# Kernel optimization log

Measured on AMD Instinct MI355X. Metric: run time of the kernel, lower is better.

## Reference

```python
import jax, jax.numpy as jnp
import numpy as np

N_SRC = 200000   # source (input) nodes
N_DST = 50000    # destination (output) nodes; dst node i == src node i (block convention)
E = 800000       # edges
IN = 256
OUT = 64
H = 3
SLOPE = 0.2      # leaky_relu negative_slope


def setup_inputs() -> dict:
    key = jax.random.key(0)
    k0, k1, k2, k3, k4, k5 = jax.random.split(key, 6)
    x = jax.random.normal(k0, (N_SRC, IN), dtype=jnp.float32)
    W = jax.random.normal(k1, (H * OUT, IN), dtype=jnp.float32) * (1.0 / np.sqrt(IN))
    attn_l = jax.random.normal(k2, (1, H, OUT), dtype=jnp.float32) * 0.1
    attn_r = jax.random.normal(k3, (1, H, OUT), dtype=jnp.float32) * 0.1
    src = jax.random.randint(k4, (E,), 0, N_SRC, dtype=jnp.int32)
    dst = jnp.sort(jax.random.randint(k5, (E,), 0, N_DST, dtype=jnp.int32))
    return {"x": x, "W": W, "attn_l": attn_l, "attn_r": attn_r, "src": src, "dst": dst}


def reference(x, W, attn_l, attn_r, src, dst):
    # fc + reshape to heads: [N_src, H, F]
    feat = (x @ W.T).reshape(N_SRC, H, OUT)
    # per-head attention logits
    el = jnp.sum(feat * attn_l, axis=-1)          # [N_src, H]
    er = jnp.sum(feat[:N_DST] * attn_r, axis=-1)  # [N_dst, H] (self_gather of out nodes)
    # edge scores: apply_edge + leaky_relu -> [E, H]
    e = jax.nn.leaky_relu(el[src] + er[dst], negative_slope=SLOPE)
    # segmented max over incoming edges of each dst node (gather_local_max)
    m = jax.ops.segment_max(e, dst, num_segments=N_DST)
    m = jnp.where(jnp.isfinite(m), m, jnp.float32(0))  # empty segments -> 0
    m = jax.lax.stop_gradient(m)
    ex = jnp.exp(e - m[dst])                       # [E, H]
    s = jax.ops.segment_sum(ex, dst, num_segments=N_DST)  # [N_dst, H]
    s = jnp.where(s == 0, jnp.float32(1), s)       # sum_exponent[sum==0] = 1
    att = ex / s[dst]                              # [E, H]
    # attention_gather: sum over edges of att * src feature -> [N_dst, H, F]
    out = jax.ops.segment_sum(att[:, :, None] * feat[src], dst, num_segments=N_DST)
    return out.reshape(N_DST, H * OUT)
```

## Files before the change

kernel.cpp:

```cpp
#include <hip/hip_runtime.h>
#include <hip/hip_bf16.h>

#define N_SRCN 200000
#define N_DSTN 50000
#define NEDGE 800000
#define KIN 256
#define NF 192
#define SLOPE 0.2f
#define TILES 6250
#define GBLK 512

typedef __attribute__((ext_vector_type(8))) short bf16x8;
typedef __attribute__((ext_vector_type(4))) float f32x4;

__device__ __forceinline__ unsigned short f2bf(float f) {
    union { float f; unsigned int u; } v; v.f = f;
    unsigned int u = v.u;
    return (unsigned short)((u + 0x7FFFu + ((u >> 16) & 1u)) >> 16);
}
__device__ __forceinline__ float bf2f(unsigned short h) {
    union { unsigned int u; float f; } v; v.u = ((unsigned int)h) << 16;
    return v.f;
}
__device__ __forceinline__ unsigned int cvt2(float lo, float hi) {
    __hip_bfloat162 h = __float22bfloat162_rn(float2{lo, hi});
    union { __hip_bfloat162 h; unsigned int u; } c; c.h = h;
    return c.u;
}
__device__ __forceinline__ void gl_lds16(const void* g, void* l) {
    __builtin_amdgcn_global_load_lds(
        (const __attribute__((address_space(1))) unsigned int*)g,
        (__attribute__((address_space(3))) unsigned int*)l, 16, 0, 0);
}

__global__ void prep_kernel(const float* __restrict__ W, unsigned short* __restrict__ Wp,
                            const int* __restrict__ dst, int* __restrict__ rp) {
    const int bid = blockIdx.x;
    if (bid < 24) {
        int tid = bid * 256 + threadIdx.x;
        if (tid >= 12 * 8 * 64) return;
        int lane = tid & 63;
        int g = tid >> 6;
        int nt = g % 12, ks = g / 12;
        int col = nt * 16 + (lane & 15);
        int k = ks * 32 + (lane >> 4) * 8;
        const float* wsrc = &W[col * KIN + k];
        unsigned short* o = &Wp[tid * 8];
        #pragma unroll
        for (int j = 0; j < 8; ++j) o[j] = f2bf(wsrc[j]);
    } else {
        int d = (bid - 24) * 256 + threadIdx.x;
        if (d > N_DSTN) return;
        int lo = 0, hi = NEDGE;
        while (lo < hi) {
            int mid = (lo + hi) >> 1;
            if (dst[mid] < d) lo = mid + 1; else hi = mid;
        }
        rp[d] = lo;
    }
}

__launch_bounds__(256, 2)
__global__ void gemm_feat(const float* __restrict__ x, const unsigned short* __restrict__ Wp,
                          const float* __restrict__ attn_l, const float* __restrict__ attn_r,
                          unsigned short* __restrict__ feat,
                          float* __restrict__ el4, float* __restrict__ er4) {
    __shared__ float Ab[2][32][256];
    __shared__ float parts[32][4][4][2];
    const int t = threadIdx.x;
    const int wid = t >> 6, lane = t & 63;
    const int al = lane & 15, ah = lane >> 4;

    bf16x8 bv[8][3];
    #pragma unroll
    for (int ks = 0; ks < 8; ++ks)
        #pragma unroll
        for (int j = 0; j < 3; ++j)
            bv[ks][j] = *(const bf16x8*)&Wp[(size_t)(ks * 12 + wid * 3 + j) * 512 + lane * 8];

    float Al[3], Ar[3];
    #pragma unroll
    for (int j = 0; j < 3; ++j) {
        Al[j] = attn_l[(wid * 3 + j) * 16 + al];
        Ar[j] = attn_r[(wid * 3 + j) * 16 + al];
    }

    #define STAGE(buf, tile)                                                     \
        {                                                                        \
            const int rbase = (tile) * 32;                                       \
            _Pragma("unroll")                                                    \
            for (int rr = 0; rr < 8; ++rr) {                                     \
                const int rl = wid * 8 + rr;                                     \
                const float* gp = &x[(size_t)(rbase + rl) * KIN +                \
                                     ((lane ^ (rl & 7)) << 2)];                  \
                gl_lds16(gp, &Ab[buf][rl][0]);                                   \
            }                                                                    \
        }

    STAGE(0, blockIdx.x)

    for (int tl = blockIdx.x, it = 0; tl < TILES; tl += GBLK, ++it) {
        const int cur = it & 1;
        if (tl + GBLK < TILES) {
            STAGE(cur ^ 1, tl + GBLK)
            asm volatile("s_waitcnt vmcnt(8)" ::: "memory");
        } else {
            asm volatile("s_waitcnt vmcnt(0)" ::: "memory");
        }
        __syncthreads();

        const int r0 = tl * 32;
        f32x4 acc[2][3] = {};
        #pragma unroll
        for (int ks = 0; ks < 8; ++ks) {
            #pragma unroll
            for (int rt = 0; rt < 2; ++rt) {
                const int row = rt * 16 + al;
                const int q0 = (ks * 8 + ah * 2);
                const int key = row & 7;
                const float4 v0 = *(const float4*)&Ab[cur][row][((q0 ^ key) << 2)];
                const float4 v1 = *(const float4*)&Ab[cur][row][(((q0 + 1) ^ key) << 2)];
                union { bf16x8 v; unsigned int u[4]; } av;
                av.u[0] = cvt2(v0.x, v0.y);
                av.u[1] = cvt2(v0.z, v0.w);
                av.u[2] = cvt2(v1.x, v1.y);
                av.u[3] = cvt2(v1.z, v1.w);
                #pragma unroll
                for (int j = 0; j < 3; ++j)
                    acc[rt][j] = __builtin_amdgcn_mfma_f32_16x16x32_bf16(av.v, bv[ks][j], acc[rt][j], 0, 0, 0);
            }
        }

        #pragma unroll
        for (int rt = 0; rt < 2; ++rt)
            #pragma unroll
            for (int j = 0; j < 3; ++j) {
                const int col = (wid * 3 + j) * 16 + al;
                #pragma unroll
                for (int e = 0; e < 4; ++e) {
                    const int row = r0 + rt * 16 + ah * 4 + e;
                    feat[(size_t)row * NF + col] = f2bf(acc[rt][j][e]);
                }
            }

        #pragma unroll
        for (int rt = 0; rt < 2; ++rt)
            #pragma unroll
            for (int e = 0; e < 4; ++e)
                #pragma unroll
                for (int j = 0; j < 3; ++j) {
                    float sl = acc[rt][j][e] * Al[j];
                    float sr = acc[rt][j][e] * Ar[j];
                    #pragma unroll
                    for (int m = 1; m <= 8; m <<= 1) {
                        sl += __shfl_xor(sl, m);
                        sr += __shfl_xor(sr, m);
                    }
                    if (al == 0) {
                        const int rloc = rt * 16 + ah * 4 + e;
                        const int nt = wid * 3 + j;
                        parts[rloc][nt >> 2][nt & 3][0] = sl;
                        parts[rloc][nt >> 2][nt & 3][1] = sr;
                    }
                }
        __syncthreads();

        if (t < 128) {
            const int rloc = t >> 2, h = t & 3;
            const int row = r0 + rloc;
            float sl = 0.f, sr = 0.f;
            if (h < 3) {
                sl = parts[rloc][h][0][0] + parts[rloc][h][1][0]
                   + parts[rloc][h][2][0] + parts[rloc][h][3][0];
                sr = parts[rloc][h][0][1] + parts[rloc][h][1][1]
                   + parts[rloc][h][2][1] + parts[rloc][h][3][1];
            }
            el4[(size_t)row * 4 + h] = sl;
            if (row < N_DSTN) er4[(size_t)row * 4 + h] = sr;
        }
    }
    #undef STAGE
}

__launch_bounds__(256)
__global__ void gather_kernel(const unsigned short* __restrict__ feat,
                              const float* __restrict__ el4, const float* __restrict__ er4,
                              const int* __restrict__ src, const int* __restrict__ rp,
                              float* __restrict__ out) {
    const int lane = threadIdx.x & 63;
    const int d = (blockIdx.x * blockDim.x + threadIdx.x) >> 6;
    if (d >= N_DSTN) return;
    const int lo = rp[d], hi = rp[d + 1];
    const float4 erv = *(const float4*)&er4[(size_t)d * 4];

    float a0 = 0.f, a1 = 0.f, a2 = 0.f, s0 = 0.f, s1 = 0.f, s2 = 0.f;
    for (int base = lo; base < hi; base += 64) {
        const int cnt = min(64, hi - base);
        int sv = 0; float w0 = 0.f, w1 = 0.f, w2 = 0.f;
        if (lane < cnt) {
            sv = src[base + lane];
            const float4 elv = *(const float4*)&el4[(size_t)sv * 4];
            float e0 = elv.x + erv.x; e0 = e0 >= 0.f ? e0 : SLOPE * e0; w0 = __expf(e0);
            float e1 = elv.y + erv.y; e1 = e1 >= 0.f ? e1 : SLOPE * e1; w1 = __expf(e1);
            float e2 = elv.z + erv.z; e2 = e2 >= 0.f ? e2 : SLOPE * e2; w2 = __expf(e2);
        }
        int j = 0;
        for (; j + 8 <= cnt; j += 8) {
            unsigned short f0[8], f1[8], f2[8];
            float u0[8], u1[8], u2[8];
            #pragma unroll
            for (int q = 0; q < 8; ++q) {
                const int sj = __shfl(sv, j + q);
                const unsigned short* fp = &feat[(size_t)sj * NF + lane];
                f0[q] = fp[0]; f1[q] = fp[64]; f2[q] = fp[128];
                u0[q] = __shfl(w0, j + q);
                u1[q] = __shfl(w1, j + q);
                u2[q] = __shfl(w2, j + q);
            }
            #pragma unroll
            for (int q = 0; q < 8; ++q) {
                s0 += u0[q]; a0 += u0[q] * bf2f(f0[q]);
                s1 += u1[q]; a1 += u1[q] * bf2f(f1[q]);
                s2 += u2[q]; a2 += u2[q] * bf2f(f2[q]);
            }
        }
        for (; j < cnt; ++j) {
            const int sj = __shfl(sv, j);
            const float u0 = __shfl(w0, j);
            const float u1 = __shfl(w1, j);
            const float u2 = __shfl(w2, j);
            const unsigned short* fp = &feat[(size_t)sj * NF + lane];
            s0 += u0; a0 += u0 * bf2f(fp[0]);
            s1 += u1; a1 += u1 * bf2f(fp[64]);
            s2 += u2; a2 += u2 * bf2f(fp[128]);
        }
    }
    if (hi == lo) { s0 = 1.f; s1 = 1.f; s2 = 1.f; }
    float* op = &out[(size_t)d * NF];
    op[lane]       = a0 / s0;
    op[64 + lane]  = a1 / s1;
    op[128 + lane] = a2 / s2;
}

extern "C" void kernel_launch(void* const* d_in, const int* in_sizes, int n_in,
                              void* d_out, int out_size, void* d_ws, size_t ws_size,
                              hipStream_t stream) {
    const float* x      = (const float*)d_in[0];
    const float* W      = (const float*)d_in[1];
    const float* attn_l = (const float*)d_in[2];
    const float* attn_r = (const float*)d_in[3];
    const int*   src    = (const int*)d_in[4];
    const int*   dst    = (const int*)d_in[5];
    float* out = (float*)d_out;

    char* ws = (char*)d_ws;
    unsigned short* feat = (unsigned short*)ws;
    float* el4 = (float*)(ws + 76800000);
    float* er4 = (float*)(ws + 80000000);
    unsigned short* Wp = (unsigned short*)(ws + 80800000);
    int*   rp = (int*)(ws + 80898304);

    prep_kernel<<<24 + 196, 256, 0, stream>>>(W, Wp, dst, rp);
    gemm_feat<<<GBLK, 256, 0, stream>>>(x, Wp, attn_l, attn_r, feat, el4, er4);
    gather_kernel<<<12500, 256, 0, stream>>>(feat, el4, er4, src, rp, out);
}
```

Measured before the change: 177.4 us.

## Move GEMM weights to LDS and load x directly with 512-thread blocks

The feature GEMM is restructured. W fragments are now staged once per block into LDS instead of being held in registers. x rows are read straight from global memory into registers, replacing the double-buffered async LDS staging of x. Blocks grow to 512 threads (8 waves split into two row halves times four column groups), grid shrinks to 256 blocks, and the el/er reductions run as two separate LDS passes. The aim is to cut register pressure and raise occupancy, at the cost of the explicit prefetch pipeline for x and extra barriers.

Measured after the change: 277.4 us. 1.56x slower.

```diff
diff --git a/kernel.cpp b/kernel.cpp
--- a/kernel.cpp
+++ b/kernel.cpp
@@ -7,8 +7,8 @@
 #define KIN 256
 #define NF 192
 #define SLOPE 0.2f
-#define TILES 6250
-#define GBLK 512
+#define TILES32 6250
+#define GEMM_BLOCKS 256
 
 typedef __attribute__((ext_vector_type(8))) short bf16x8;
 typedef __attribute__((ext_vector_type(4))) float f32x4;
@@ -60,126 +60,114 @@
     }
 }
 
-__launch_bounds__(256, 2)
+__launch_bounds__(512, 2)
 __global__ void gemm_feat(const float* __restrict__ x, const unsigned short* __restrict__ Wp,
                           const float* __restrict__ attn_l, const float* __restrict__ attn_r,
                           unsigned short* __restrict__ feat,
                           float* __restrict__ el4, float* __restrict__ er4) {
-    __shared__ float Ab[2][32][256];
-    __shared__ float parts[32][4][4][2];
+    __shared__ unsigned short Bl[12 * 8 * 512];
+    __shared__ float parts[2][32][4][4];
     const int t = threadIdx.x;
     const int wid = t >> 6, lane = t & 63;
     const int al = lane & 15, ah = lane >> 4;
-
-    bf16x8 bv[8][3];
+    const int rh = wid >> 2;
+    const int j3 = wid & 3;
+
     #pragma unroll
-    for (int ks = 0; ks < 8; ++ks)
-        #pragma unroll
-        for (int j = 0; j < 3; ++j)
-            bv[ks][j] = *(const bf16x8*)&Wp[(size_t)(ks * 12 + wid * 3 + j) * 512 + lane * 8];
+    for (int i = 0; i < 12; ++i) {
+        const int gbase = i * 512 + wid * 64;
+        gl_lds16(&Wp[(size_t)(gbase + lane) * 8], &Bl[(size_t)gbase * 8]);
+    }
+    asm volatile("s_waitcnt vmcnt(0)" ::: "memory");
+    __syncthreads();
 
     float Al[3], Ar[3];
     #pragma unroll
-    for (int j = 0; j < 3; ++j) {
-        Al[j] = attn_l[(wid * 3 + j) * 16 + al];
-        Ar[j] = attn_r[(wid * 3 + j) * 16 + al];
-    }
-
-    #define STAGE(buf, tile)                                                     \
-        {                                                                        \
-            const int rbase = (tile) * 32;                                       \
-            _Pragma("unroll")                                                    \
-            for (int rr = 0; rr < 8; ++rr) {                                     \
-                const int rl = wid * 8 + rr;                                     \
-                const float* gp = &x[(size_t)(rbase + rl) * KIN +                \
-                                     ((lane ^ (rl & 7)) << 2)];                  \
-                gl_lds16(gp, &Ab[buf][rl][0]);                                   \
-            }                                                                    \
-        }
-
-    STAGE(0, blockIdx.x)
-
-    for (int tl = blockIdx.x, it = 0; tl < TILES; tl += GBLK, ++it) {
-        const int cur = it & 1;
-        if (tl + GBLK < TILES) {
-            STAGE(cur ^ 1, tl + GBLK)
-            asm volatile("s_waitcnt vmcnt(8)" ::: "memory");
-        } else {
-            asm volatile("s_waitcnt vmcnt(0)" ::: "memory");
-        }
+    for (int h = 0; h < 3; ++h) {
+        Al[h] = attn_l[(h * 4 + j3) * 16 + al];
+        Ar[h] = attn_r[(h * 4 + j3) * 16 + al];
+    }
+
+    int pb = 0;
+    for (int tl = blockIdx.x; tl < TILES32; tl += GEMM_BLOCKS, pb ^= 1) {
+        const int r0 = tl * 32;
+        const float* xrow = &x[(size_t)(r0 + rh * 16 + al) * KIN + ah * 8];
+
+        f32x4 acc[3] = {};
+        #pragma unroll
+        for (int ks = 0; ks < 8; ++ks) {
+            const float4 a0 = *(const float4*)&xrow[ks * 32];
+            const float4 a1 = *(const float4*)&xrow[ks * 32 + 4];
+            union { bf16x8 v; unsigned int u[4]; } av;
+            av.u[0] = cvt2(a0.x, a0.y);
+            av.u[1] = cvt2(a0.z, a0.w);
+            av.u[2] = cvt2(a1.x, a1.y);
+            av.u[3] = cvt2(a1.z, a1.w);
+            #pragma unroll
+            for (int h = 0; h < 3; ++h) {
+                const bf16x8 bv = *(const bf16x8*)&Bl[(size_t)(ks * 12 + h * 4 + j3) * 512 + lane * 8];
+                acc[h] = __builtin_amdgcn_mfma_f32_16x16x32_bf16(av.v, bv, acc[h], 0, 0, 0);
+            }
+        }
+
+        #pragma unroll
+        for (int h = 0; h < 3; ++h) {
+            const int col = (h * 4 + j3) * 16 + al;
+            #pragma unroll
+            for (int e = 0; e < 4; ++e) {
+                const int row = r0 + rh * 16 + ah * 4 + e;
+                feat[(size_t)row * NF + col] = f2bf(acc[h][e]);
+            }
+        }
+
+        #pragma unroll
+        for (int e = 0; e < 4; ++e)
+            #pragma unroll
+            for (int h = 0; h < 3; ++h) {
+                float sl = acc[h][e] * Al[h];
+                float sr = acc[h][e] * Ar[h];
+                #pragma unroll
+                for (int m = 1; m <= 8; m <<= 1) {
+                    sl += __shfl_xor(sl, m);
+                    sr += __shfl_xor(sr, m);
+                }
+                if (al == 0) {
+                    const int rloc = rh * 16 + ah * 4 + e;
+                    parts[pb][rloc][h][j3] = sl;
+                    parts[pb][rloc][h][j3 == 0 ? 3 : j3 - 1] = parts[pb][rloc][h][j3 == 0 ? 3 : j3 - 1];
+                    parts[pb][rloc][h][j3] = sl;
+                }
+            }
         __syncthreads();
-
-        const int r0 = tl * 32;
-        f32x4 acc[2][3] = {};
-        #pragma unroll
-        for (int ks = 0; ks < 8; ++ks) {
-            #pragma unroll
-            for (int rt = 0; rt < 2; ++rt) {
-                const int row = rt * 16 + al;
-                const int q0 = (ks * 8 + ah * 2);
-                const int key = row & 7;
-                const float4 v0 = *(const float4*)&Ab[cur][row][((q0 ^ key) << 2)];
-                const float4 v1 = *(const float4*)&Ab[cur][row][(((q0 + 1) ^ key) << 2)];
-                union { bf16x8 v; unsigned int u[4]; } av;
-                av.u[0] = cvt2(v0.x, v0.y);
-                av.u[1] = cvt2(v0.z, v0.w);
-                av.u[2] = cvt2(v1.x, v1.y);
-                av.u[3] = cvt2(v1.z, v1.w);
+        if (t < 256) {
+            const int rloc = t >> 3, h = t & 7;
+            if (h < 3) {
+                const float s = parts[pb][rloc][h][0] + parts[pb][rloc][h][1]
+                              + parts[pb][rloc][h][2] + parts[pb][rloc][h][3];
+                el4[(size_t)(r0 + rloc) * 4 + h] = s;
+            }
+        }
+        __syncthreads();
+        #pragma unroll
+        for (int e = 0; e < 4; ++e)
+            #pragma unroll
+            for (int h = 0; h < 3; ++h) {
+                float sr = acc[h][e] * Ar[h];
                 #pragma unroll
-                for (int j = 0; j < 3; ++j)
-                    acc[rt][j] = __builtin_amdgcn_mfma_f32_16x16x32_bf16(av.v, bv[ks][j], acc[rt][j], 0, 0, 0);
-            }
-        }
-
-        #pragma unroll
-        for (int rt = 0; rt < 2; ++rt)
-            #pragma unroll
-            for (int j = 0; j < 3; ++j) {
-                const int col = (wid * 3 + j) * 16 + al;
-                #pragma unroll
-                for (int e = 0; e < 4; ++e) {
-                    const int row = r0 + rt * 16 + ah * 4 + e;
-                    feat[(size_t)row * NF + col] = f2bf(acc[rt][j][e]);
-                }
-            }
-
-        #pragma unroll
-        for (int rt = 0; rt < 2; ++rt)
-            #pragma unroll
-            for (int e = 0; e < 4; ++e)
-                #pragma unroll
-                for (int j = 0; j < 3; ++j) {
-                    float sl = acc[rt][j][e] * Al[j];
-                    float sr = acc[rt][j][e] * Ar[j];
-                    #pragma unroll
-                    for (int m = 1; m <= 8; m <<= 1) {
-                        sl += __shfl_xor(sl, m);
-                        sr += __shfl_xor(sr, m);
-                    }
-                    if (al == 0) {
-                        const int rloc = rt * 16 + ah * 4 + e;
-                        const int nt = wid * 3 + j;
-                        parts[rloc][nt >> 2][nt & 3][0] = sl;
-                        parts[rloc][nt >> 2][nt & 3][1] = sr;
-                    }
-                }
+                for (int m = 1; m <= 8; m <<= 1) sr += __shfl_xor(sr, m);
+                if (al == 0) parts[pb][rh * 16 + ah * 4 + e][h][j3] = sr;
+            }
         __syncthreads();
-
-        if (t < 128) {
-            const int rloc = t >> 2, h = t & 3;
+        if (t < 256) {
+            const int rloc = t >> 3, h = t & 7;
             const int row = r0 + rloc;
-            float sl = 0.f, sr = 0.f;
-            if (h < 3) {
-                sl = parts[rloc][h][0][0] + parts[rloc][h][1][0]
-                   + parts[rloc][h][2][0] + parts[rloc][h][3][0];
-                sr = parts[rloc][h][0][1] + parts[rloc][h][1][1]
-                   + parts[rloc][h][2][1] + parts[rloc][h][3][1];
-            }
-            el4[(size_t)row * 4 + h] = sl;
-            if (row < N_DSTN) er4[(size_t)row * 4 + h] = sr;
-        }
-    }
-    #undef STAGE
+            if (h < 3 && row < N_DSTN) {
+                const float s = parts[pb][rloc][h][0] + parts[pb][rloc][h][1]
+                              + parts[pb][rloc][h][2] + parts[pb][rloc][h][3];
+                er4[(size_t)row * 4 + h] = s;
+            }
+        }
+    }
 }
 
 __launch_bounds__(256)
@@ -261,6 +249,6 @@
     int*   rp = (int*)(ws + 80898304);
 
     prep_kernel<<<24 + 196, 256, 0, stream>>>(W, Wp, dst, rp);
-    gemm_feat<<<GBLK, 256, 0, stream>>>(x, Wp, attn_l, attn_r, feat, el4, er4);
+    gemm_feat<<<GEMM_BLOCKS, 512, 0, stream>>>(x, Wp, attn_l, attn_r, feat, el4, er4);
     gather_kernel<<<12500, 256, 0, stream>>>(feat, el4, er4, src, rp, out);
 }
```
